# Optimization experiments

Hardware: AMD Instinct MI355X
Metric: run time of the kernel (lower is better)

## Reference

```python
import jax, jax.numpy as jnp
import numpy as np

N_NODES = 100000
HIDDEN = 128
IN_FEAT = 128
N_EDGES = 600000


def setup_inputs() -> dict:
    key = jax.random.key(0)
    ks = jax.random.split(key, 8)
    x = jax.random.normal(ks[0], (N_NODES, IN_FEAT), dtype=jnp.float32)
    edge_index = jax.random.randint(ks[1], (2, N_EDGES), 0, N_NODES, dtype=jnp.int64)
    # Glorot-style init for the three GCNConv layers (in->hidden, hidden->hidden, hidden->hidden)
    s_in = 1.0 / np.sqrt(IN_FEAT)
    s_h = 1.0 / np.sqrt(HIDDEN)
    W1 = jax.random.normal(ks[2], (IN_FEAT, HIDDEN), dtype=jnp.float32) * s_in
    b1 = jnp.zeros((HIDDEN,), dtype=jnp.float32)
    W2 = jax.random.normal(ks[3], (HIDDEN, HIDDEN), dtype=jnp.float32) * s_h
    b2 = jnp.zeros((HIDDEN,), dtype=jnp.float32)
    W3 = jax.random.normal(ks[4], (HIDDEN, HIDDEN), dtype=jnp.float32) * s_h
    b3 = jnp.zeros((HIDDEN,), dtype=jnp.float32)
    return {"x": x, "W1": W1, "b1": b1, "W2": W2, "b2": b2, "W3": W3, "b3": b3,
            "edge_index": edge_index}


def _gcn_conv(x, W, b, row, col, norm, n_nodes):
    # GCNConv (add_self_loops=False): out = D^{-1/2} A D^{-1/2} (x W) + b
    h = x @ W                                   # [N, H]
    msg = h[row] * norm[:, None]                # gather sources, scale per edge [E, H]
    agg = jax.ops.segment_sum(msg, col, num_segments=n_nodes)  # scatter-add to targets
    return agg + b


def reference(x, W1, b1, W2, b2, W3, b3, edge_index):
    row, col = edge_index[0], edge_index[1]
    # Symmetric GCN normalization, no self loops, unit edge weights.
    deg = jax.ops.segment_sum(jnp.ones(row.shape[0], dtype=x.dtype), col,
                              num_segments=N_NODES)
    deg_inv_sqrt = jnp.where(deg > 0, jax.lax.rsqrt(jnp.maximum(deg, 1.0)), 0.0)
    norm = deg_inv_sqrt[row] * deg_inv_sqrt[col]  # [E]

    h = _gcn_conv(x, W1, b1, row, col, norm, N_NODES)
    h = jax.nn.relu(h)  # dropout(p=0.1) is identity in eval mode
    h = _gcn_conv(h, W2, b2, row, col, norm, N_NODES)
    h = jax.nn.relu(h)
    h = _gcn_conv(h, W3, b3, row, col, norm, N_NODES)
    return h
```

## Files before the change

kernel.cpp:

```cpp
#include <hip/hip_runtime.h>
#include <cstddef>

#define NN 100000
#define NE 600000
#define HID 128

typedef _Float16 half8 __attribute__((ext_vector_type(8)));
typedef _Float16 half2v __attribute__((ext_vector_type(2)));
typedef float f32x4 __attribute__((ext_vector_type(4)));

union H8 { _Float16 h[8]; half2v p[4]; uint4 u; half8 v; };

__global__ void k_degi(const int* __restrict__ col, int* __restrict__ degi, int E) {
    int e = blockIdx.x * blockDim.x + threadIdx.x;
    if (e < E) atomicAdd(&degi[col[e]], 1);
}

__global__ void k_wprep(const float* __restrict__ W1, const float* __restrict__ W2,
                        const float* __restrict__ W3, _Float16* __restrict__ wt) {
    int b = blockIdx.x;
    int layer = b >> 7, k = b & 127;
    const float* W = layer == 0 ? W1 : (layer == 1 ? W2 : W3);
    int c = threadIdx.x;
    wt[((size_t)layer << 14) + c * 128 + k] = (_Float16)W[k * 128 + c];
}

__global__ void k_blocksum(const int* __restrict__ degi, float* __restrict__ dinv,
                           int* __restrict__ bsum, int N) {
    __shared__ int sh[256];
    int i = blockIdx.x * 256 + threadIdx.x;
    int v = i < N ? degi[i] : 0;
    if (i < N) dinv[i] = v > 0 ? rsqrtf((float)v) : 0.0f;
    sh[threadIdx.x] = v;
    __syncthreads();
    for (int s = 128; s > 0; s >>= 1) {
        if (threadIdx.x < s) sh[threadIdx.x] += sh[threadIdx.x + s];
        __syncthreads();
    }
    if (threadIdx.x == 0) bsum[blockIdx.x] = sh[0];
}

__global__ void k_scan_bsum(int* __restrict__ bsum, int nb) {
    __shared__ int sh[512];
    int tid = threadIdx.x;
    int v = (tid < nb) ? bsum[tid] : 0;
    sh[tid] = v;
    __syncthreads();
    #pragma unroll
    for (int s = 1; s < 512; s <<= 1) {
        int t = (tid >= s) ? sh[tid - s] : 0;
        __syncthreads();
        sh[tid] += t;
        __syncthreads();
    }
    if (tid < nb) bsum[tid] = sh[tid] - v;
}

__global__ void k_scan_apply(const int* __restrict__ degi, const int* __restrict__ bsum,
                             int* __restrict__ rowptr, int* __restrict__ cursor, int N) {
    __shared__ int sh[256];
    int i = blockIdx.x * 256 + threadIdx.x;
    int v = (i < N) ? degi[i] : 0;
    sh[threadIdx.x] = v;
    __syncthreads();
    #pragma unroll
    for (int s = 1; s < 256; s <<= 1) {
        int t = (threadIdx.x >= s) ? sh[threadIdx.x - s] : 0;
        __syncthreads();
        sh[threadIdx.x] += t;
        __syncthreads();
    }
    if (i < N) {
        int excl = bsum[blockIdx.x] + sh[threadIdx.x] - v;
        rowptr[i] = excl;
        cursor[i] = excl;
        if (i == N - 1) rowptr[N] = bsum[blockIdx.x] + sh[threadIdx.x];
    }
}

__global__ void k_fill_csr(const int* __restrict__ row, const int* __restrict__ col,
                           int* __restrict__ cursor, int* __restrict__ csr_off, int E) {
    int e = blockIdx.x * blockDim.x + threadIdx.x;
    if (e >= E) return;
    int r = row[e], c = col[e];
    int pos = atomicAdd(&cursor[c], 1);
    csr_off[pos] = r * (HID * 2);
}

template <typename TA>
__global__ __launch_bounds__(256, 2) void k_gemm(
    const TA* __restrict__ A, const _Float16* __restrict__ WT,
    const float* __restrict__ dinv, _Float16* __restrict__ H, int nrows)
{
    __shared__ _Float16 asl[128 * 128];
    __shared__ _Float16 wsl[128 * 128];
    const int tid  = threadIdx.x;
    const int lane = tid & 63;
    const int w    = tid >> 6;
    const int wm   = w >> 1, wn = w & 1;
    const int ln15 = lane & 15;
    const int hi   = lane >> 4;
    const int row0 = blockIdx.x * 128;

    #pragma unroll
    for (int i = 0; i < 8; ++i) {
        int g = i * 256 + tid;
        int c = g >> 4, k8 = (g & 15) << 3;
        uint4 wv = *(const uint4*)(WT + c * 128 + k8);
        *(uint4*)&wsl[c * 128 + (k8 ^ ((c & 7) << 3))] = wv;
    }
    #pragma unroll
    for (int i = 0; i < 8; ++i) {
        int g = i * 256 + tid;
        int r = g >> 4, c8 = (g & 15) << 3;
        int gr = row0 + r; if (gr >= nrows) gr = nrows - 1;
        if constexpr (sizeof(TA) == 4) {
            const float4* src = (const float4*)(A + (size_t)gr * HID + c8);
            float4 v0 = src[0], v1 = src[1];
            H8 o;
            o.h[0] = (_Float16)v0.x; o.h[1] = (_Float16)v0.y;
            o.h[2] = (_Float16)v0.z; o.h[3] = (_Float16)v0.w;
            o.h[4] = (_Float16)v1.x; o.h[5] = (_Float16)v1.y;
            o.h[6] = (_Float16)v1.z; o.h[7] = (_Float16)v1.w;
            *(uint4*)&asl[r * 128 + (c8 ^ ((r & 7) << 3))] = o.u;
        } else {
            uint4 u = *(const uint4*)(A + (size_t)gr * HID + c8);
            *(uint4*)&asl[r * 128 + (c8 ^ ((r & 7) << 3))] = u;
        }
    }
    __syncthreads();

    f32x4 acc[4][4];
    #pragma unroll
    for (int i = 0; i < 4; ++i)
        #pragma unroll
        for (int j = 0; j < 4; ++j) {
            acc[i][j][0] = 0.0f; acc[i][j][1] = 0.0f;
            acc[i][j][2] = 0.0f; acc[i][j][3] = 0.0f;
        }

    #pragma unroll
    for (int ks = 0; ks < 4; ++ks) {
        const int k0 = ks * 32 + hi * 8;
        half8 a[4], b[4];
        #pragma unroll
        for (int i = 0; i < 4; ++i) {
            int ra = wm * 64 + i * 16 + ln15;
            a[i] = *(const half8*)&asl[ra * 128 + (k0 ^ ((ra & 7) << 3))];
            int cb = wn * 64 + i * 16 + ln15;
            b[i] = *(const half8*)&wsl[cb * 128 + (k0 ^ ((cb & 7) << 3))];
        }
        #pragma unroll
        for (int i = 0; i < 4; ++i)
            #pragma unroll
            for (int j = 0; j < 4; ++j)
                acc[i][j] = __builtin_amdgcn_mfma_f32_16x16x32_f16(a[i], b[j], acc[i][j], 0, 0, 0);
    }

    #pragma unroll
    for (int i = 0; i < 4; ++i) {
        #pragma unroll
        for (int q = 0; q < 4; ++q) {
            int r = row0 + wm * 64 + i * 16 + hi * 4 + q;
            if (r < nrows) {
                float s = dinv[r];
                #pragma unroll
                for (int j = 0; j < 4; ++j) {
                    H[(size_t)r * HID + wn * 64 + j * 16 + ln15] =
                        (_Float16)(acc[i][j][q] * s);
                }
            }
        }
    }
}

template <int MODE>
__global__ __launch_bounds__(256) void k_aggregate(
    const _Float16* __restrict__ hs, const int* __restrict__ csr_off,
    const int* __restrict__ rowptr, const float* __restrict__ dinv,
    const float* __restrict__ bias, void* __restrict__ aggv, int N)
{
    constexpr int NB = 32;
    constexpr int CAP = 2048;
    __shared__ int s_off[CAP + 8];
    __shared__ int s_ptr[NB + 1];

    const int tid = threadIdx.x;
    const int n0  = blockIdx.x * NB;
    if (tid <= NB) s_ptr[tid] = rowptr[n0 + tid];
    __syncthreads();
    const int Rbeg = s_ptr[0];
    const int cnt  = s_ptr[NB] - Rbeg;
    const bool fast = cnt <= CAP;
    if (fast) {
        for (int i = tid; i < cnt; i += 256) s_off[i] = csr_off[Rbeg + i];
    }
    __syncthreads();
    const int* offp = fast ? (const int*)s_off : (csr_off + Rbeg);

    const int lane = tid & 63;
    const int w    = tid >> 6;
    const int es   = lane >> 4;
    const int fg   = lane & 15;
    const char* hb = (const char*)hs;
    const int f0   = fg * 8 + es * 2;
    const float2 bv = *(const float2*)(bias + f0);

#if __has_builtin(__builtin_amdgcn_fdot2)
    const half2v selx = {(_Float16)1.0f, (_Float16)0.0f};
    const half2v sely = {(_Float16)0.0f, (_Float16)1.0f};
#define ACC8(hh)                                                              \
    do {                                                                      \
        _Pragma("unroll")                                                     \
        for (int p = 0; p < 4; ++p) {                                         \
            accf[2*p]   = __builtin_amdgcn_fdot2((hh).p[p], selx, accf[2*p],   false); \
            accf[2*p+1] = __builtin_amdgcn_fdot2((hh).p[p], sely, accf[2*p+1], false); \
        }                                                                     \
    } while (0)
#else
#define ACC8(hh)                                                              \
    do {                                                                      \
        _Pragma("unroll")                                                     \
        for (int j = 0; j < 8; ++j) accf[j] += (float)(hh).h[j];              \
    } while (0)
#endif

    #pragma unroll 2
    for (int t = 0; t < 8; ++t) {
        const int ni   = (w << 3) + t;
        const int node = n0 + ni;
        const int beg  = s_ptr[ni] - Rbeg;
        const int end  = s_ptr[ni + 1] - Rbeg;

        float accf[8];
        #pragma unroll
        for (int j = 0; j < 8; ++j) accf[j] = 0.0f;

        const uint4 z = make_uint4(0, 0, 0, 0);
        int nr  = (end - beg + 3) >> 2;
        int idx = beg + es;
        int r   = 0;
        for (; r + 1 < nr; r += 2, idx += 8) {
            int o0 = (idx     < end) ? offp[idx]     : -1;
            int o1 = (idx + 4 < end) ? offp[idx + 4] : -1;
            uint4 u0 = (o0 >= 0) ? *(const uint4*)(hb + (size_t)(unsigned)o0 + fg * 16) : z;
            uint4 u1 = (o1 >= 0) ? *(const uint4*)(hb + (size_t)(unsigned)o1 + fg * 16) : z;
            H8 h0; h0.u = u0;
            H8 h1; h1.u = u1;
            ACC8(h0);
            ACC8(h1);
        }
        if (r < nr) {
            int o0 = (idx < end) ? offp[idx] : -1;
            uint4 u0 = (o0 >= 0) ? *(const uint4*)(hb + (size_t)(unsigned)o0 + fg * 16) : z;
            H8 h0; h0.u = u0;
            ACC8(h0);
        }

        #pragma unroll
        for (int j = 0; j < 8; ++j) {
            accf[j] += __shfl_xor(accf[j], 16);
            accf[j] += __shfl_xor(accf[j], 32);
        }

        float v0 = es < 2 ? (es == 0 ? accf[0] : accf[2])
                          : (es == 2 ? accf[4] : accf[6]);
        float v1 = es < 2 ? (es == 0 ? accf[1] : accf[3])
                          : (es == 2 ? accf[5] : accf[7]);
        float s = dinv[node];
        v0 = v0 * s + bv.x;
        v1 = v1 * s + bv.y;
        if constexpr (MODE == 0) {
            union { _Float16 h[2]; unsigned u; } o;
            o.h[0] = (_Float16)fmaxf(v0, 0.0f);
            o.h[1] = (_Float16)fmaxf(v1, 0.0f);
            *(unsigned*)((_Float16*)aggv + (size_t)node * HID + f0) = o.u;
        } else {
            *(float2*)((float*)aggv + (size_t)node * HID + f0) = make_float2(v0, v1);
        }
    }
#undef ACC8
}

extern "C" void kernel_launch(void* const* d_in, const int* in_sizes, int n_in,
                              void* d_out, int out_size, void* d_ws, size_t ws_size,
                              hipStream_t stream)
{
    const float* x  = (const float*)d_in[0];
    const float* W1 = (const float*)d_in[1];
    const float* b1 = (const float*)d_in[2];
    const float* W2 = (const float*)d_in[3];
    const float* b2 = (const float*)d_in[4];
    const float* W3 = (const float*)d_in[5];
    const float* b3 = (const float*)d_in[6];
    const int*   ei = (const int*)d_in[7];
    const int* row  = ei;
    const int* colv = ei + NE;
    float* out = (float*)d_out;

    _Float16* h16 = (_Float16*)d_ws;
    _Float16* a16 = h16 + (size_t)NN * HID;
    _Float16* wt  = a16 + (size_t)NN * HID;
    int*   degi    = (int*)(wt + 3 * 128 * 128);
    float* dinv    = (float*)(degi + NN);
    int*   rowptr  = (int*)(dinv + NN);
    int*   cursor  = rowptr + NN + 1;
    int*   bsum    = cursor + NN;
    int*   csr_off = bsum + 512;

    const int TB = 256;
    const int nScanBlocks = (NN + 255) / 256;

    k_wprep<<<384, 128, 0, stream>>>(W1, W2, W3, wt);
    hipMemsetAsync(degi, 0, NN * sizeof(int), stream);
    k_degi      <<<(NE + TB - 1) / TB, TB, 0, stream>>>(colv, degi, NE);
    k_blocksum  <<<nScanBlocks, 256, 0, stream>>>(degi, dinv, bsum, NN);
    k_scan_bsum <<<1, 512, 0, stream>>>(bsum, nScanBlocks);
    k_scan_apply<<<nScanBlocks, 256, 0, stream>>>(degi, bsum, rowptr, cursor, NN);
    k_fill_csr  <<<(NE + TB - 1) / TB, TB, 0, stream>>>(row, colv, cursor, csr_off, NE);

    const int gemmBlocks = (NN + 127) / 128;
    const int aggBlocks  = (NN + 31) / 32;

    k_gemm<float><<<gemmBlocks, TB, 0, stream>>>(x, wt, dinv, h16, NN);
    k_aggregate<0><<<aggBlocks, TB, 0, stream>>>(h16, csr_off, rowptr, dinv, b1, a16, NN);
    k_gemm<_Float16><<<gemmBlocks, TB, 0, stream>>>(a16, wt + (1 << 14), dinv, h16, NN);
    k_aggregate<0><<<aggBlocks, TB, 0, stream>>>(h16, csr_off, rowptr, dinv, b2, a16, NN);
    k_gemm<_Float16><<<gemmBlocks, TB, 0, stream>>>(a16, wt + (2 << 14), dinv, h16, NN);
    k_aggregate<1><<<aggBlocks, TB, 0, stream>>>(h16, csr_off, rowptr, dinv, b3, out, NN);
}
```

Before: 247.9 us.

## Fuse aggregation of layers 1 and 2 into the following GEMM kernel

Merges the aggregate-plus-ReLU of layers 1 and 2 into the next layer's GEMM. Each block gathers neighbor features for its 128 rows straight into shared memory as the A tile, then runs MFMA against the next weight matrix. This removes two launches and the fp16 write and read of the intermediate activations. In exchange, each block now runs a long serial gather of 32 nodes per wave before its GEMM, occupancy is limited by 64KB of shared memory, and CSR offsets are read from global memory instead of being staged in LDS.

```diff
diff --git a/kernel.cpp b/kernel.cpp
--- a/kernel.cpp
+++ b/kernel.cpp
@@ -10,6 +10,21 @@
 typedef float f32x4 __attribute__((ext_vector_type(4)));
 
 union H8 { _Float16 h[8]; half2v p[4]; uint4 u; half8 v; };
+
+__device__ __forceinline__ void acc8(const H8& hh, float* accf) {
+#if __has_builtin(__builtin_amdgcn_fdot2)
+    const half2v selx = {(_Float16)1.0f, (_Float16)0.0f};
+    const half2v sely = {(_Float16)0.0f, (_Float16)1.0f};
+    #pragma unroll
+    for (int p = 0; p < 4; ++p) {
+        accf[2*p]   = __builtin_amdgcn_fdot2(hh.p[p], selx, accf[2*p],   false);
+        accf[2*p+1] = __builtin_amdgcn_fdot2(hh.p[p], sely, accf[2*p+1], false);
+    }
+#else
+    #pragma unroll
+    for (int j = 0; j < 8; ++j) accf[j] += (float)hh.h[j];
+#endif
+}
 
 __global__ void k_degi(const int* __restrict__ col, int* __restrict__ degi, int E) {
     int e = blockIdx.x * blockDim.x + threadIdx.x;
@@ -87,9 +102,8 @@
     csr_off[pos] = r * (HID * 2);
 }
 
-template <typename TA>
 __global__ __launch_bounds__(256, 2) void k_gemm(
-    const TA* __restrict__ A, const _Float16* __restrict__ WT,
+    const float* __restrict__ A, const _Float16* __restrict__ WT,
     const float* __restrict__ dinv, _Float16* __restrict__ H, int nrows)
 {
     __shared__ _Float16 asl[128 * 128];
@@ -114,19 +128,14 @@
         int g = i * 256 + tid;
         int r = g >> 4, c8 = (g & 15) << 3;
         int gr = row0 + r; if (gr >= nrows) gr = nrows - 1;
-        if constexpr (sizeof(TA) == 4) {
-            const float4* src = (const float4*)(A + (size_t)gr * HID + c8);
-            float4 v0 = src[0], v1 = src[1];
-            H8 o;
-            o.h[0] = (_Float16)v0.x; o.h[1] = (_Float16)v0.y;
-            o.h[2] = (_Float16)v0.z; o.h[3] = (_Float16)v0.w;
-            o.h[4] = (_Float16)v1.x; o.h[5] = (_Float16)v1.y;
-            o.h[6] = (_Float16)v1.z; o.h[7] = (_Float16)v1.w;
-            *(uint4*)&asl[r * 128 + (c8 ^ ((r & 7) << 3))] = o.u;
-        } else {
-            uint4 u = *(const uint4*)(A + (size_t)gr * HID + c8);
-            *(uint4*)&asl[r * 128 + (c8 ^ ((r & 7) << 3))] = u;
-        }
+        const float4* src = (const float4*)(A + (size_t)gr * HID + c8);
+        float4 v0 = src[0], v1 = src[1];
+        H8 o;
+        o.h[0] = (_Float16)v0.x; o.h[1] = (_Float16)v0.y;
+        o.h[2] = (_Float16)v0.z; o.h[3] = (_Float16)v0.w;
+        o.h[4] = (_Float16)v1.x; o.h[5] = (_Float16)v1.y;
+        o.h[6] = (_Float16)v1.z; o.h[7] = (_Float16)v1.w;
+        *(uint4*)&asl[r * 128 + (c8 ^ ((r & 7) << 3))] = o.u;
     }
     __syncthreads();
 
@@ -174,11 +183,140 @@
     }
 }
 
-template <int MODE>
-__global__ __launch_bounds__(256) void k_aggregate(
+__global__ __launch_bounds__(256, 2) void k_gemm_agg(
+    const _Float16* __restrict__ hprev, const int* __restrict__ csr_off,
+    const int* __restrict__ rowptr, const float* __restrict__ dinv,
+    const float* __restrict__ bias, const _Float16* __restrict__ WT,
+    _Float16* __restrict__ H, int nrows)
+{
+    __shared__ _Float16 asl[128 * 128];
+    __shared__ _Float16 wsl[128 * 128];
+    __shared__ int s_ptr[129];
+    const int tid  = threadIdx.x;
+    const int lane = tid & 63;
+    const int w    = tid >> 6;
+    const int row0 = blockIdx.x * 128;
+
+    if (tid < 129) {
+        int n = row0 + tid; if (n > nrows) n = nrows;
+        s_ptr[tid] = rowptr[n];
+    }
+    #pragma unroll
+    for (int i = 0; i < 8; ++i) {
+        int g = i * 256 + tid;
+        int c = g >> 4, k8 = (g & 15) << 3;
+        uint4 wv = *(const uint4*)(WT + c * 128 + k8);
+        *(uint4*)&wsl[c * 128 + (k8 ^ ((c & 7) << 3))] = wv;
+    }
+    __syncthreads();
+
+    const int es = lane >> 4;
+    const int fg = lane & 15;
+    const char* hb = (const char*)hprev;
+    const int f0 = fg * 8 + es * 2;
+    const float2 bv = *(const float2*)(bias + f0);
+    const uint4 z = make_uint4(0, 0, 0, 0);
+
+    #pragma unroll 2
+    for (int t = 0; t < 32; ++t) {
+        const int ni  = (w << 5) + t;
+        const int beg = s_ptr[ni], end = s_ptr[ni + 1];
+
+        float accf[8];
+        #pragma unroll
+        for (int j = 0; j < 8; ++j) accf[j] = 0.0f;
+
+        int nr  = (end - beg + 3) >> 2;
+        int idx = beg + es;
+        int r   = 0;
+        for (; r + 1 < nr; r += 2, idx += 8) {
+            int o0 = (idx     < end) ? csr_off[idx]     : -1;
+            int o1 = (idx + 4 < end) ? csr_off[idx + 4] : -1;
+            uint4 u0 = (o0 >= 0) ? *(const uint4*)(hb + (size_t)(unsigned)o0 + fg * 16) : z;
+            uint4 u1 = (o1 >= 0) ? *(const uint4*)(hb + (size_t)(unsigned)o1 + fg * 16) : z;
+            H8 h0; h0.u = u0;
+            H8 h1; h1.u = u1;
+            acc8(h0, accf);
+            acc8(h1, accf);
+        }
+        if (r < nr) {
+            int o0 = (idx < end) ? csr_off[idx] : -1;
+            uint4 u0 = (o0 >= 0) ? *(const uint4*)(hb + (size_t)(unsigned)o0 + fg * 16) : z;
+            H8 h0; h0.u = u0;
+            acc8(h0, accf);
+        }
+
+        #pragma unroll
+        for (int j = 0; j < 8; ++j) {
+            accf[j] += __shfl_xor(accf[j], 16);
+            accf[j] += __shfl_xor(accf[j], 32);
+        }
+
+        float v0 = es < 2 ? (es == 0 ? accf[0] : accf[2])
+                          : (es == 2 ? accf[4] : accf[6]);
+        float v1 = es < 2 ? (es == 0 ? accf[1] : accf[3])
+                          : (es == 2 ? accf[5] : accf[7]);
+        int node = row0 + ni;
+        float s = (node < nrows) ? dinv[node] : 0.0f;
+        union { _Float16 h[2]; unsigned u; } o;
+        o.h[0] = (_Float16)fmaxf(v0 * s + bv.x, 0.0f);
+        o.h[1] = (_Float16)fmaxf(v1 * s + bv.y, 0.0f);
+        *(unsigned*)&asl[ni * 128 + (((unsigned)(fg * 8)) ^ ((ni & 7) << 3)) + es * 2] = o.u;
+    }
+    __syncthreads();
+
+    const int wm   = w >> 1, wn = w & 1;
+    const int ln15 = lane & 15;
+    const int hi   = lane >> 4;
+
+    f32x4 acc[4][4];
+    #pragma unroll
+    for (int i = 0; i < 4; ++i)
+        #pragma unroll
+        for (int j = 0; j < 4; ++j) {
+            acc[i][j][0] = 0.0f; acc[i][j][1] = 0.0f;
+            acc[i][j][2] = 0.0f; acc[i][j][3] = 0.0f;
+        }
+
+    #pragma unroll
+    for (int ks = 0; ks < 4; ++ks) {
+        const int k0 = ks * 32 + hi * 8;
+        half8 a[4], b[4];
+        #pragma unroll
+        for (int i = 0; i < 4; ++i) {
+            int ra = wm * 64 + i * 16 + ln15;
+            a[i] = *(const half8*)&asl[ra * 128 + (k0 ^ ((ra & 7) << 3))];
+            int cb = wn * 64 + i * 16 + ln15;
+            b[i] = *(const half8*)&wsl[cb * 128 + (k0 ^ ((cb & 7) << 3))];
+        }
+        #pragma unroll
+        for (int i = 0; i < 4; ++i)
+            #pragma unroll
+            for (int j = 0; j < 4; ++j)
+                acc[i][j] = __builtin_amdgcn_mfma_f32_16x16x32_f16(a[i], b[j], acc[i][j], 0, 0, 0);
+    }
+
+    #pragma unroll
+    for (int i = 0; i < 4; ++i) {
+        #pragma unroll
+        for (int q = 0; q < 4; ++q) {
+            int r = row0 + wm * 64 + i * 16 + hi * 4 + q;
+            if (r < nrows) {
+                float s = dinv[r];
+                #pragma unroll
+                for (int j = 0; j < 4; ++j) {
+                    H[(size_t)r * HID + wn * 64 + j * 16 + ln15] =
+                        (_Float16)(acc[i][j][q] * s);
+                }
+            }
+        }
+    }
+}
+
+__global__ __launch_bounds__(256) void k_aggregate_f(
     const _Float16* __restrict__ hs, const int* __restrict__ csr_off,
     const int* __restrict__ rowptr, const float* __restrict__ dinv,
-    const float* __restrict__ bias, void* __restrict__ aggv, int N)
+    const float* __restrict__ bias, float* __restrict__ out, int N)
 {
     constexpr int NB = 32;
     constexpr int CAP = 2048;
@@ -205,25 +343,7 @@
     const char* hb = (const char*)hs;
     const int f0   = fg * 8 + es * 2;
     const float2 bv = *(const float2*)(bias + f0);
-
-#if __has_builtin(__builtin_amdgcn_fdot2)
-    const half2v selx = {(_Float16)1.0f, (_Float16)0.0f};
-    const half2v sely = {(_Float16)0.0f, (_Float16)1.0f};
-#define ACC8(hh)                                                              \
-    do {                                                                      \
-        _Pragma("unroll")                                                     \
-        for (int p = 0; p < 4; ++p) {                                         \
-            accf[2*p]   = __builtin_amdgcn_fdot2((hh).p[p], selx, accf[2*p],   false); \
-            accf[2*p+1] = __builtin_amdgcn_fdot2((hh).p[p], sely, accf[2*p+1], false); \
-        }                                                                     \
-    } while (0)
-#else
-#define ACC8(hh)                                                              \
-    do {                                                                      \
-        _Pragma("unroll")                                                     \
-        for (int j = 0; j < 8; ++j) accf[j] += (float)(hh).h[j];              \
-    } while (0)
-#endif
+    const uint4 z = make_uint4(0, 0, 0, 0);
 
     #pragma unroll 2
     for (int t = 0; t < 8; ++t) {
@@ -236,7 +356,6 @@
         #pragma unroll
         for (int j = 0; j < 8; ++j) accf[j] = 0.0f;
 
-        const uint4 z = make_uint4(0, 0, 0, 0);
         int nr  = (end - beg + 3) >> 2;
         int idx = beg + es;
         int r   = 0;
@@ -247,14 +366,14 @@
             uint4 u1 = (o1 >= 0) ? *(const uint4*)(hb + (size_t)(unsigned)o1 + fg * 16) : z;
             H8 h0; h0.u = u0;
             H8 h1; h1.u = u1;
-            ACC8(h0);
-            ACC8(h1);
+            acc8(h0, accf);
+            acc8(h1, accf);
         }
         if (r < nr) {
             int o0 = (idx < end) ? offp[idx] : -1;
             uint4 u0 = (o0 >= 0) ? *(const uint4*)(hb + (size_t)(unsigned)o0 + fg * 16) : z;
             H8 h0; h0.u = u0;
-            ACC8(h0);
+            acc8(h0, accf);
         }
 
         #pragma unroll
@@ -270,16 +389,8 @@
         float s = dinv[node];
         v0 = v0 * s + bv.x;
         v1 = v1 * s + bv.y;
-        if constexpr (MODE == 0) {
-            union { _Float16 h[2]; unsigned u; } o;
-            o.h[0] = (_Float16)fmaxf(v0, 0.0f);
-            o.h[1] = (_Float16)fmaxf(v1, 0.0f);
-            *(unsigned*)((_Float16*)aggv + (size_t)node * HID + f0) = o.u;
-        } else {
-            *(float2*)((float*)aggv + (size_t)node * HID + f0) = make_float2(v0, v1);
-        }
-    }
-#undef ACC8
+        *(float2*)(out + (size_t)node * HID + f0) = make_float2(v0, v1);
+    }
 }
 
 extern "C" void kernel_launch(void* const* d_in, const int* in_sizes, int n_in,
@@ -298,9 +409,9 @@
     const int* colv = ei + NE;
     float* out = (float*)d_out;
 
-    _Float16* h16 = (_Float16*)d_ws;
-    _Float16* a16 = h16 + (size_t)NN * HID;
-    _Float16* wt  = a16 + (size_t)NN * HID;
+    _Float16* hA  = (_Float16*)d_ws;
+    _Float16* hB  = hA + (size_t)NN * HID;
+    _Float16* wt  = hB + (size_t)NN * HID;
     int*   degi    = (int*)(wt + 3 * 128 * 128);
     float* dinv    = (float*)(degi + NN);
     int*   rowptr  = (int*)(dinv + NN);
@@ -322,10 +433,10 @@
     const int gemmBlocks = (NN + 127) / 128;
     const int aggBlocks  = (NN + 31) / 32;
 
-    k_gemm<float><<<gemmBlocks, TB, 0, stream>>>(x, wt, dinv, h16, NN);
-    k_aggregate<0><<<aggBlocks, TB, 0, stream>>>(h16, csr_off, rowptr, dinv, b1, a16, NN);
-    k_gemm<_Float16><<<gemmBlocks, TB, 0, stream>>>(a16, wt + (1 << 14), dinv, h16, NN);
-    k_aggregate<0><<<aggBlocks, TB, 0, stream>>>(h16, csr_off, rowptr, dinv, b2, a16, NN);
-    k_gemm<_Float16><<<gemmBlocks, TB, 0, stream>>>(a16, wt + (2 << 14), dinv, h16, NN);
-    k_aggregate<1><<<aggBlocks, TB, 0, stream>>>(h16, csr_off, rowptr, dinv, b3, out, NN);
-}
+    k_gemm<<<gemmBlocks, TB, 0, stream>>>(x, wt, dinv, hA, NN);
+    k_gemm_agg<<<gemmBlocks, TB, 0, stream>>>(hA, csr_off, rowptr, dinv, b1,
+                                              wt + (1 << 14), hB, NN);
+    k_gemm_agg<<<gemmBlocks, TB, 0, stream>>>(hB, csr_off, rowptr, dinv, b2,
+                                              wt + (2 << 14), hA, NN);
+    k_aggregate_f<<<aggBlocks, TB, 0, stream>>>(hA, csr_off, rowptr, dinv, b3, out, NN);
+}
```

Result: slower. 323.7 us (+30.6%).
